# Performance work log

Hardware: AMD Instinct MI355X
Metric: run time of the kernel (lower is better)

## Reference

```python
import jax, jax.numpy as jnp
import numpy as np

B, T, E, H = 4, 2048, 1024, 16
D = E // H

def setup_inputs() -> dict:
    key = jax.random.key(0)
    ks = jax.random.split(key, 8)
    s = 0.02
    return {
        "q": jax.random.normal(ks[0], (B, T, E), dtype=jnp.float32),
        "k": jax.random.normal(ks[1], (B, T, E), dtype=jnp.float32),
        "v": jax.random.normal(ks[2], (B, T, E), dtype=jnp.float32),
        "Wq": jax.random.normal(ks[3], (E, E), dtype=jnp.float32) * s,
        "Wk": jax.random.normal(ks[4], (E, E), dtype=jnp.float32) * s,
        "Wv": jax.random.normal(ks[5], (E, E), dtype=jnp.float32) * s,
        "Wp": jax.random.normal(ks[6], (E, E), dtype=jnp.float32) * s,
        "bp": jnp.zeros((E,), dtype=jnp.float32),
    }

def reference(q, k, v, Wq, Wk, Wv, Wp, bp):
    # Linear projections (torch Linear: x @ W.T). NOTE: original code computes
    # key from the already-projected query (k = self.key(q)); external k is unused.
    qp = q @ Wq.T                      # [B,T,E]
    kp = qp @ Wk.T                     # [B,T,E]  <- faithful quirk
    vp = v @ Wv.T                      # [B,T,E]
    qh = qp.reshape(B, T, H, D).transpose(0, 2, 1, 3)  # [B,H,T,D]
    kh = kp.reshape(B, T, H, D).transpose(0, 2, 1, 3)
    vh = vp.reshape(B, T, H, D).transpose(0, 2, 1, 3)
    # Faithful quirk: att = scores / D**(-1/2) == scores * sqrt(D)
    scale = jnp.float32(D) ** 0.5
    att = jnp.einsum('bhtd,bhsd->bhts', qh, kh) * scale  # [B,H,T,T]
    causal = jnp.tril(jnp.ones((T, T), dtype=bool))
    att = jnp.where(causal, att, -jnp.inf)
    att = jax.nn.softmax(att, axis=-1)
    y = jnp.einsum('bhts,bhsd->bhtd', att, vh)           # [B,H,T,D]
    y = y.transpose(0, 2, 1, 3).reshape(B, T, E)
    return y @ Wp.T + bp
```

## Files before the change

kernel.cpp:

```cpp
#include <hip/hip_runtime.h>


typedef unsigned short u16;
typedef unsigned int   u32;
typedef __attribute__((ext_vector_type(8))) __bf16 bf16x8;
typedef __attribute__((ext_vector_type(8))) u16    u16x8;
typedef __attribute__((ext_vector_type(4))) u16    u16x4;
typedef __attribute__((ext_vector_type(4))) float  f32x4;
typedef __attribute__((ext_vector_type(4))) int    i32x4;

#define DEV static __device__ __forceinline__

DEV u16 f2bf(float x){ union{float f;u32 u;}v; v.f=x; u32 r=v.u+0x7fffu+((v.u>>16)&1u); return (u16)(r>>16); }
DEV float bf2f(u16 b){ union{u32 u;float f;}v; v.u=((u32)b)<<16; return v.f; }
DEV f32x4 zero4(){ f32x4 z={0.f,0.f,0.f,0.f}; return z; }
DEV f32x4 mfma16(bf16x8 a, bf16x8 b, f32x4 c){ return __builtin_amdgcn_mfma_f32_16x16x32_bf16(a,b,c,0,0,0); }
DEV void gld16(const u16* g, u16* l){
  __builtin_amdgcn_global_load_lds((const __attribute__((address_space(1))) u32*)g,
                                   (__attribute__((address_space(3))) u32*)l, 16, 0, 0);
}
DEV u32 pkbf(float a, float b){
  union{float f;u32 u;}x,y; x.f=a; y.f=b;
  return __builtin_amdgcn_perm(y.u+0x8000u, x.u+0x8000u, 0x07060302u);
}

constexpr int B_=4, T_=2048, E_=1024;
constexpr int M_=B_*T_;
constexpr float L2E8 = 11.5415603f;

__global__ __launch_bounds__(256)
void cvt_a(const float* __restrict__ q, const float* __restrict__ v,
           u16* __restrict__ qi, u16* __restrict__ vb)
{
  const int j=blockIdx.y;
  const size_t e=((size_t)blockIdx.x*256+threadIdx.x)*8;
  const float* s=(j==0)?q:v;
  f32x4 x0=*reinterpret_cast<const f32x4*>(s+e);
  f32x4 x1=*reinterpret_cast<const f32x4*>(s+e+4);
  u16x8 h,l;
#pragma unroll
  for(int t=0;t<4;t++){
    u16 hh=f2bf(x0[t]); h[t]=hh; l[t]=f2bf(x0[t]-bf2f(hh));
    u16 h2=f2bf(x1[t]); h[t+4]=h2; l[t+4]=f2bf(x1[t]-bf2f(h2));
  }
  if(j==0){
    const size_t row=e>>10, k=e&1023;
    u16* d=qi + row*2048 + (k>>3)*16;
    *reinterpret_cast<u16x8*>(d)=h;
    *reinterpret_cast<u16x8*>(d+8)=l;
  } else {
    *reinterpret_cast<u16x8*>(vb+e)=h;
  }
}

__global__ __launch_bounds__(256)
void cvt_w(const float* __restrict__ Wq, const float* __restrict__ Wk, const float* __restrict__ Wv,
           u16* __restrict__ wqi, u16* __restrict__ wki, u16* __restrict__ wvb)
{
  const int j=blockIdx.y;
  const size_t e=((size_t)blockIdx.x*256+threadIdx.x)*8;
  const float* s=(j==0)?Wq:(j==1)?Wk:Wv;
  f32x4 x0=*reinterpret_cast<const f32x4*>(s+e);
  f32x4 x1=*reinterpret_cast<const f32x4*>(s+e+4);
  u16x8 h,l;
#pragma unroll
  for(int t=0;t<4;t++){
    u16 hh=f2bf(x0[t]); h[t]=hh; l[t]=f2bf(x0[t]-bf2f(hh));
    u16 h2=f2bf(x1[t]); h[t+4]=h2; l[t+4]=f2bf(x1[t]-bf2f(h2));
  }
  if(j==2){ *reinterpret_cast<u16x8*>(wvb+e)=h; return; }
  u16* base=(j==0)?wqi:wki;
  const size_t row=e>>10, k=e&1023;
  u16* d=base + row*2048 + (k>>3)*16;
  *reinterpret_cast<u16x8*>(d)=h;
  *reinterpret_cast<u16x8*>(d+8)=l;
}

__global__ __launch_bounds__(256)
void cvt_p(const float* __restrict__ Wp, u16* __restrict__ wpb)
{
  const size_t e=((size_t)blockIdx.x*256+threadIdx.x)*8;
  f32x4 x0=*reinterpret_cast<const f32x4*>(Wp+e);
  f32x4 x1=*reinterpret_cast<const f32x4*>(Wp+e+4);
  u16x8 h;
#pragma unroll
  for(int t=0;t<4;t++){ h[t]=f2bf(x0[t]); h[t+4]=f2bf(x1[t]); }
  *reinterpret_cast<u16x8*>(wpb+e)=h;
}

template<int SPLIT,int OMODE>
__global__ __launch_bounds__(256)
void gemm(const u16* __restrict__ Ag, const u16* __restrict__ Bg,
          const float* __restrict__ bias,
          u16* __restrict__ Ob, float* __restrict__ Of, int ldc)
{
  __shared__ u16 sA[SPLIT?128*128:128*64];
  __shared__ u16 sB[SPLIT?128*128:128*64];

  const int tid=threadIdx.x, wave=tid>>6, lane=tid&63;
  const int quad=lane>>4, l16=lane&15, sw=l16&7;
  const int wm=(wave>>1)*64, wn=(wave&1)*64;
  const int n0=blockIdx.x*128, m0=blockIdx.y*128;

  f32x4 acc[4][4];
#pragma unroll
  for(int i=0;i<4;i++)
#pragma unroll
    for(int j=0;j<4;j++) acc[i][j]=zero4();

  for(int k0=0;k0<E_;k0+=64){
    if(SPLIT){
#pragma unroll
      for(int it=0;it<8;it++){
        const int c=it*256+tid, row=c>>4, j=(c&15)^(row&7);
        gld16(Ag + (size_t)(m0+row)*2048 + k0*2 + j*8, &sA[(it*256+wave*64)*8]);
      }
#pragma unroll
      for(int it=0;it<8;it++){
        const int c=it*256+tid, row=c>>4, j=(c&15)^(row&7);
        gld16(Bg + (size_t)(n0+row)*2048 + k0*2 + j*8, &sB[(it*256+wave*64)*8]);
      }
    } else {
#pragma unroll
      for(int it=0;it<4;it++){
        const int c=it*256+tid, row=c>>3, j=(c&7)^(row&7);
        gld16(Ag + (size_t)(m0+row)*1024 + k0 + j*8, &sA[(it*256+wave*64)*8]);
      }
#pragma unroll
      for(int it=0;it<4;it++){
        const int c=it*256+tid, row=c>>3, j=(c&7)^(row&7);
        gld16(Bg + (size_t)(n0+row)*1024 + k0 + j*8, &sB[(it*256+wave*64)*8]);
      }
    }
    __syncthreads();

#pragma unroll
    for(int kk=0;kk<2;kk++){
      if(SPLIT){
        bf16x8 ahh[4],ahl[4],bhh[4],bhl[4];
#pragma unroll
        for(int i=0;i<4;i++){
          const u16* pa=&sA[(wm+i*16+l16)*128];
          const u16* pb=&sB[(wn+i*16+l16)*128];
          const int ch=2*(kk*4+quad);
          ahh[i]=*reinterpret_cast<const bf16x8*>(&pa[((ch  )^sw)*8]);
          ahl[i]=*reinterpret_cast<const bf16x8*>(&pa[((ch+1)^sw)*8]);
          bhh[i]=*reinterpret_cast<const bf16x8*>(&pb[((ch  )^sw)*8]);
          bhl[i]=*reinterpret_cast<const bf16x8*>(&pb[((ch+1)^sw)*8]);
        }
#pragma unroll
        for(int i=0;i<4;i++)
#pragma unroll
          for(int j=0;j<4;j++){
            acc[i][j]=mfma16(ahh[i],bhh[j],acc[i][j]);
            acc[i][j]=mfma16(ahh[i],bhl[j],acc[i][j]);
            acc[i][j]=mfma16(ahl[i],bhh[j],acc[i][j]);
          }
      } else {
        bf16x8 a[4],b[4];
#pragma unroll
        for(int i=0;i<4;i++){
          a[i]=*reinterpret_cast<const bf16x8*>(&sA[(wm+i*16+l16)*64 + (((kk*4+quad)^sw)*8)]);
          b[i]=*reinterpret_cast<const bf16x8*>(&sB[(wn+i*16+l16)*64 + (((kk*4+quad)^sw)*8)]);
        }
#pragma unroll
        for(int i=0;i<4;i++)
#pragma unroll
          for(int j=0;j<4;j++)
            acc[i][j]=mfma16(a[i],b[j],acc[i][j]);
      }
    }
    __syncthreads();
  }

#pragma unroll
  for(int i=0;i<4;i++)
#pragma unroll
    for(int j=0;j<4;j++){
      const int col=n0+wn+j*16+l16;
#pragma unroll
      for(int r=0;r<4;r++){
        const int row=m0+wm+i*16+quad*4+r;
        float v=acc[i][j][r];
        if(OMODE==2)      Of[(size_t)row*ldc+col]=v+bias[col];
        else if(OMODE==1) Ob[(size_t)row*ldc+col]=f2bf(v);
        else {
          u16 hh=f2bf(v);
          const size_t base=(size_t)row*2048 + (size_t)(col>>3)*16 + (col&7);
          Ob[base]=hh; Ob[base+8]=f2bf(v-bf2f(hh));
        }
      }
    }
}

__global__ __launch_bounds__(256)
void attn(const u16* __restrict__ qpi, const u16* __restrict__ kpi,
          const u16* __restrict__ vpT, u16* __restrict__ yout)
{
  __shared__ u16 sK [64*128];
  __shared__ u16 sVT[64*64];

  const int tid=threadIdx.x, wave=tid>>6, lane=tid&63;
  const int quad=lane>>4, l16=lane&15, sw=l16&7;
  const int qt=(int)(gridDim.x-1-blockIdx.x)>>6;
  const int bh=blockIdx.x&63;
  const int b=bh>>4, h=bh&15;
  const int qr0=qt*128+wave*32;

  bf16x8 qfh[2][2], qfl[2][2];
#pragma unroll
  for(int mt=0;mt<2;mt++)
#pragma unroll
    for(int ksv=0;ksv<2;ksv++){
      const size_t off=(size_t)(b*T_+qr0+mt*16+l16)*2048 + h*128 + (ksv*4+quad)*16;
      qfh[mt][ksv]=*reinterpret_cast<const bf16x8*>(qpi+off);
      qfl[mt][ksv]=*reinterpret_cast<const bf16x8*>(qpi+off+8);
    }

  float mst[2]={-1e30f,-1e30f}, lst[2]={0.f,0.f};
  f32x4 oacc[2][4];
#pragma unroll
  for(int mt=0;mt<2;mt++)
#pragma unroll
    for(int dt=0;dt<4;dt++) oacc[mt][dt]=zero4();

  const int nkt=2*(qt+1);
  for(int kt=0;kt<nkt;kt++){
    const int s0=kt*64;
    __syncthreads();
#pragma unroll
    for(int it=0;it<4;it++){
      const int c=it*256+tid, row=c>>4, j=(c&15)^(row&7);
      gld16(kpi + (size_t)(b*T_+s0+row)*2048 + h*128 + j*8,
            &sK[(it*256+wave*64)*8]);
    }
#pragma unroll
    for(int it=0;it<2;it++){
      const int c=it*256+tid, row=c>>3, j=(c&7)^(row&7);
      gld16(vpT + (size_t)(h*64+row)*8192 + b*T_ + s0 + j*8,
            &sVT[(it*256+wave*64)*8]);
    }
    __syncthreads();

    if(s0<=qr0+31){
      f32x4 sacc[4][2];
#pragma unroll
      for(int st=0;st<4;st++)
#pragma unroll
        for(int mt=0;mt<2;mt++) sacc[st][mt]=zero4();
#pragma unroll
      for(int st=0;st<4;st++)
#pragma unroll
        for(int ksv=0;ksv<2;ksv++){
          const u16* pk=&sK[(st*16+l16)*128];
          const int ch=2*(ksv*4+quad);
          bf16x8 kh=*reinterpret_cast<const bf16x8*>(&pk[((ch  )^sw)*8]);
          bf16x8 kl=*reinterpret_cast<const bf16x8*>(&pk[((ch+1)^sw)*8]);
#pragma unroll
          for(int mt=0;mt<2;mt++){
            sacc[st][mt]=mfma16(kh,qfh[mt][ksv],sacc[st][mt]);
            sacc[st][mt]=mfma16(kl,qfh[mt][ksv],sacc[st][mt]);
            sacc[st][mt]=mfma16(kh,qfl[mt][ksv],sacc[st][mt]);
          }
        }
      const bool needmask=(s0+63>qr0);
      u32 pk_[4][2][2];
#pragma unroll
      for(int mt=0;mt<2;mt++){
        const int qrow=qr0+mt*16+l16;
        float mloc=-1e30f;
#pragma unroll
        for(int st=0;st<4;st++)
#pragma unroll
          for(int r=0;r<4;r++){
            float v=sacc[st][mt][r];
            if(needmask && (s0+st*16+quad*4+r>qrow)) v=-1e30f;
            sacc[st][mt][r]=v;
            mloc=fmaxf(mloc,v);
          }
        mloc=fmaxf(mloc,__shfl_xor(mloc,16,64));
        mloc=fmaxf(mloc,__shfl_xor(mloc,32,64));
        const float nm=fmaxf(mst[mt],mloc);
        const float alpha=exp2f((mst[mt]-nm)*L2E8);
        mst[mt]=nm;
        const float cexp=nm*L2E8;
        float rs=0.f;
#pragma unroll
        for(int st=0;st<4;st++)
#pragma unroll
          for(int r=0;r<4;r++){
            float p=exp2f(__builtin_fmaf(sacc[st][mt][r],L2E8,-cexp));
            sacc[st][mt][r]=p;
            rs+=p;
          }
        lst[mt]=lst[mt]*alpha+rs;
#pragma unroll
        for(int dt=0;dt<4;dt++) oacc[mt][dt]*=alpha;
#pragma unroll
        for(int st=0;st<4;st++){
          pk_[st][mt][0]=pkbf(sacc[st][mt][0],sacc[st][mt][1]);
          pk_[st][mt][1]=pkbf(sacc[st][mt][2],sacc[st][mt][3]);
        }
      }
      const int srcA=(2*(quad&1))*16+l16, srcB=srcA+16;
      const bool hs=(quad>=2);
#pragma unroll
      for(int ksv=0;ksv<2;ksv++){
        bf16x8 b2[2];
#pragma unroll
        for(int mt=0;mt<2;mt++){
          int e0=__shfl((int)pk_[2*ksv  ][mt][0],srcA,64);
          int g0=__shfl((int)pk_[2*ksv+1][mt][0],srcA,64);
          int e1=__shfl((int)pk_[2*ksv  ][mt][1],srcA,64);
          int g1=__shfl((int)pk_[2*ksv+1][mt][1],srcA,64);
          int e2=__shfl((int)pk_[2*ksv  ][mt][0],srcB,64);
          int g2=__shfl((int)pk_[2*ksv+1][mt][0],srcB,64);
          int e3=__shfl((int)pk_[2*ksv  ][mt][1],srcB,64);
          int g3=__shfl((int)pk_[2*ksv+1][mt][1],srcB,64);
          i32x4 bd={ hs?g0:e0, hs?g1:e1, hs?g2:e2, hs?g3:e3 };
          b2[mt]=*reinterpret_cast<bf16x8*>(&bd);
        }
#pragma unroll
        for(int dt=0;dt<4;dt++){
          bf16x8 va=*reinterpret_cast<const bf16x8*>(&sVT[(dt*16+l16)*64 + (((ksv*4+quad)^sw)*8)]);
#pragma unroll
          for(int mt=0;mt<2;mt++)
            oacc[mt][dt]=mfma16(va,b2[mt],oacc[mt][dt]);
        }
      }
    }
  }
#pragma unroll
  for(int mt=0;mt<2;mt++){
    float lt=lst[mt];
    lt+=__shfl_xor(lt,16,64);
    lt+=__shfl_xor(lt,32,64);
    const float inv=1.0f/lt;
    const size_t rb=(size_t)(b*T_+qr0+mt*16+l16)*1024 + h*64;
#pragma unroll
    for(int dt=0;dt<4;dt++){
      u16x4 o4;
#pragma unroll
      for(int r=0;r<4;r++) o4[r]=f2bf(oacc[mt][dt][r]*inv);
      *reinterpret_cast<u16x4*>(yout + rb + dt*16 + quad*4)=o4;
    }
  }
}

extern "C" void kernel_launch(void* const* d_in, const int* in_sizes, int n_in,
                              void* d_out, int out_size, void* d_ws, size_t ws_size,
                              hipStream_t stream)
{
  const float* q =(const float*)d_in[0];
  const float* v =(const float*)d_in[2];
  const float* Wq=(const float*)d_in[3];
  const float* Wk=(const float*)d_in[4];
  const float* Wv=(const float*)d_in[5];
  const float* Wp=(const float*)d_in[6];
  const float* bp=(const float*)d_in[7];
  float* out=(float*)d_out;

  const size_t NE=(size_t)M_*E_;
  const size_t WE=(size_t)E_*E_;
  u16* wsv=(u16*)d_ws;
  u16* qsl_i=wsv;
  u16* qp_i =wsv+2*NE;
  u16* kp_i =wsv;
  u16* wp_b =wsv+2*NE;
  u16* vpT  =wsv+4*NE;
  u16* ybf  =wsv+5*NE;
  u16* og   =(u16*)d_out;
  u16* wq_i =og;
  u16* wk_i =og+2*WE;
  u16* wv_b =og+4*WE;
  u16* vb   =og+5*WE;

  dim3 blk(256);
  cvt_a<<<dim3(NE/2048,2), blk, 0, stream>>>(q, v, qsl_i, vb);
  cvt_w<<<dim3(WE/2048,3), blk, 0, stream>>>(Wq, Wk, Wv, wq_i, wk_i, wv_b);

  dim3 g(E_/128, M_/128);
  gemm<1,0><<<g, blk, 0, stream>>>(qsl_i, wq_i, nullptr, qp_i, nullptr, 0);
  gemm<1,0><<<g, blk, 0, stream>>>(qp_i, wk_i, nullptr, kp_i, nullptr, 0);
  gemm<0,1><<<dim3(M_/128, E_/128), blk, 0, stream>>>(wv_b, vb, nullptr, vpT, nullptr, M_);
  attn<<<dim3(1024), blk, 0, stream>>>(qp_i, kp_i, vpT, ybf);
  cvt_p<<<dim3(WE/2048), blk, 0, stream>>>(Wp, wp_b);
  gemm<0,2><<<g, blk, 0, stream>>>(ybf, wp_b, bp, nullptr, out, E_);
}
```

Before: 437.8 us.

## Double-buffer attention K/V tiles, pair causal q-tiles, lazy softmax rescale

The attention kernel now double-buffers the K and V^T tiles in LDS and prefetches the next tile while the current one is computed, with one barrier per iteration instead of two. Each block handles two query tiles (pr and 15-pr) to balance the causal work, so the grid is halved to 512 blocks. The online-softmax rescale is skipped when the new max exceeds the running max by at most 1.0, MFMA sections are wrapped in s_setprio, and bf16 packing uses the hardware v_cvt_pk_bf16_f32. Doubled LDS may reduce occupancy, and the lazy-rescale threshold slightly changes numerics.

```diff
diff --git a/kernel.cpp b/kernel.cpp
--- a/kernel.cpp
+++ b/kernel.cpp
@@ -19,9 +19,10 @@
   __builtin_amdgcn_global_load_lds((const __attribute__((address_space(1))) u32*)g,
                                    (__attribute__((address_space(3))) u32*)l, 16, 0, 0);
 }
-DEV u32 pkbf(float a, float b){
-  union{float f;u32 u;}x,y; x.f=a; y.f=b;
-  return __builtin_amdgcn_perm(y.u+0x8000u, x.u+0x8000u, 0x07060302u);
+DEV u32 cvtpk(float lo, float hi){
+  u32 r;
+  asm("v_cvt_pk_bf16_f32 %0, %1, %2" : "=v"(r) : "v"(lo), "v"(hi));
+  return r;
 }
 
 constexpr int B_=4, T_=2048, E_=1024;
@@ -197,152 +198,176 @@
 void attn(const u16* __restrict__ qpi, const u16* __restrict__ kpi,
           const u16* __restrict__ vpT, u16* __restrict__ yout)
 {
-  __shared__ u16 sK [64*128];
-  __shared__ u16 sVT[64*64];
+  __shared__ u16 sK [2][64*128];
+  __shared__ u16 sVT[2][64*64];
 
   const int tid=threadIdx.x, wave=tid>>6, lane=tid&63;
   const int quad=lane>>4, l16=lane&15, sw=l16&7;
-  const int qt=(int)(gridDim.x-1-blockIdx.x)>>6;
+  const int pr=(int)blockIdx.x>>6;
   const int bh=blockIdx.x&63;
   const int b=bh>>4, h=bh&15;
-  const int qr0=qt*128+wave*32;
-
-  bf16x8 qfh[2][2], qfl[2][2];
-#pragma unroll
-  for(int mt=0;mt<2;mt++)
-#pragma unroll
-    for(int ksv=0;ksv<2;ksv++){
-      const size_t off=(size_t)(b*T_+qr0+mt*16+l16)*2048 + h*128 + (ksv*4+quad)*16;
-      qfh[mt][ksv]=*reinterpret_cast<const bf16x8*>(qpi+off);
-      qfl[mt][ksv]=*reinterpret_cast<const bf16x8*>(qpi+off+8);
-    }
-
-  float mst[2]={-1e30f,-1e30f}, lst[2]={0.f,0.f};
-  f32x4 oacc[2][4];
-#pragma unroll
-  for(int mt=0;mt<2;mt++)
-#pragma unroll
-    for(int dt=0;dt<4;dt++) oacc[mt][dt]=zero4();
-
-  const int nkt=2*(qt+1);
-  for(int kt=0;kt<nkt;kt++){
-    const int s0=kt*64;
-    __syncthreads();
+
+  auto STAGE=[&](int buf, int kt2){
+    const int s0=kt2*64;
 #pragma unroll
     for(int it=0;it<4;it++){
       const int c=it*256+tid, row=c>>4, j=(c&15)^(row&7);
       gld16(kpi + (size_t)(b*T_+s0+row)*2048 + h*128 + j*8,
-            &sK[(it*256+wave*64)*8]);
+            &sK[buf][(it*256+wave*64)*8]);
     }
 #pragma unroll
     for(int it=0;it<2;it++){
       const int c=it*256+tid, row=c>>3, j=(c&7)^(row&7);
       gld16(vpT + (size_t)(h*64+row)*8192 + b*T_ + s0 + j*8,
-            &sVT[(it*256+wave*64)*8]);
-    }
+            &sVT[buf][(it*256+wave*64)*8]);
+    }
+  };
+
+#pragma unroll 1
+  for(int half=0; half<2; half++){
+    const int qt = half ? (15-pr) : pr;
+    const int qr0=qt*128+wave*32;
+
+    bf16x8 qfh[2][2], qfl[2][2];
+#pragma unroll
+    for(int mt=0;mt<2;mt++)
+#pragma unroll
+      for(int ksv=0;ksv<2;ksv++){
+        const size_t off=(size_t)(b*T_+qr0+mt*16+l16)*2048 + h*128 + (ksv*4+quad)*16;
+        qfh[mt][ksv]=*reinterpret_cast<const bf16x8*>(qpi+off);
+        qfl[mt][ksv]=*reinterpret_cast<const bf16x8*>(qpi+off+8);
+      }
+
+    float mst[2]={-1e30f,-1e30f}, lst[2]={0.f,0.f};
+    f32x4 oacc[2][4];
+#pragma unroll
+    for(int mt=0;mt<2;mt++)
+#pragma unroll
+      for(int dt=0;dt<4;dt++) oacc[mt][dt]=zero4();
+
+    const int nkt=2*(qt+1);
+    STAGE(0, 0);
     __syncthreads();
 
-    if(s0<=qr0+31){
-      f32x4 sacc[4][2];
-#pragma unroll
-      for(int st=0;st<4;st++)
-#pragma unroll
-        for(int mt=0;mt<2;mt++) sacc[st][mt]=zero4();
-#pragma unroll
-      for(int st=0;st<4;st++)
+    for(int kt=0;kt<nkt;kt++){
+      const int cur=kt&1;
+      if(kt+1<nkt) STAGE(cur^1, kt+1);
+      const int s0=kt*64;
+
+      if(s0<=qr0+31){
+        f32x4 sacc[4][2];
+#pragma unroll
+        for(int st=0;st<4;st++)
+#pragma unroll
+          for(int mt=0;mt<2;mt++) sacc[st][mt]=zero4();
+        __builtin_amdgcn_s_setprio(1);
+#pragma unroll
+        for(int st=0;st<4;st++)
+#pragma unroll
+          for(int ksv=0;ksv<2;ksv++){
+            const u16* pk=&sK[cur][(st*16+l16)*128];
+            const int ch=2*(ksv*4+quad);
+            bf16x8 kh=*reinterpret_cast<const bf16x8*>(&pk[((ch  )^sw)*8]);
+            bf16x8 kl=*reinterpret_cast<const bf16x8*>(&pk[((ch+1)^sw)*8]);
+#pragma unroll
+            for(int mt=0;mt<2;mt++){
+              sacc[st][mt]=mfma16(kh,qfh[mt][ksv],sacc[st][mt]);
+              sacc[st][mt]=mfma16(kl,qfh[mt][ksv],sacc[st][mt]);
+              sacc[st][mt]=mfma16(kh,qfl[mt][ksv],sacc[st][mt]);
+            }
+          }
+        __builtin_amdgcn_s_setprio(0);
+        const bool needmask=(s0+63>qr0);
+        u32 pk_[4][2][2];
+#pragma unroll
+        for(int mt=0;mt<2;mt++){
+          const int qrow=qr0+mt*16+l16;
+          float mloc=-1e30f;
+#pragma unroll
+          for(int st=0;st<4;st++)
+#pragma unroll
+            for(int r=0;r<4;r++){
+              float v=sacc[st][mt][r];
+              if(needmask && (s0+st*16+quad*4+r>qrow)) v=-1e30f;
+              sacc[st][mt][r]=v;
+              mloc=fmaxf(mloc,v);
+            }
+          mloc=fmaxf(mloc,__shfl_xor(mloc,16,64));
+          mloc=fmaxf(mloc,__shfl_xor(mloc,32,64));
+          float cexp;
+          if(__all(mloc <= mst[mt]+1.0f)){
+            cexp=mst[mt]*L2E8;
+          } else {
+            const float nm=fmaxf(mst[mt],mloc);
+            const float alpha=exp2f((mst[mt]-nm)*L2E8);
+            mst[mt]=nm;
+            lst[mt]*=alpha;
+#pragma unroll
+            for(int dt=0;dt<4;dt++) oacc[mt][dt]*=alpha;
+            cexp=nm*L2E8;
+          }
+          float rs=0.f;
+#pragma unroll
+          for(int st=0;st<4;st++)
+#pragma unroll
+            for(int r=0;r<4;r++){
+              float p=exp2f(__builtin_fmaf(sacc[st][mt][r],L2E8,-cexp));
+              sacc[st][mt][r]=p;
+              rs+=p;
+            }
+          lst[mt]+=rs;
+#pragma unroll
+          for(int st=0;st<4;st++){
+            pk_[st][mt][0]=cvtpk(sacc[st][mt][0],sacc[st][mt][1]);
+            pk_[st][mt][1]=cvtpk(sacc[st][mt][2],sacc[st][mt][3]);
+          }
+        }
+        const int srcA=(2*(quad&1))*16+l16, srcB=srcA+16;
+        const bool hs=(quad>=2);
 #pragma unroll
         for(int ksv=0;ksv<2;ksv++){
-          const u16* pk=&sK[(st*16+l16)*128];
-          const int ch=2*(ksv*4+quad);
-          bf16x8 kh=*reinterpret_cast<const bf16x8*>(&pk[((ch  )^sw)*8]);
-          bf16x8 kl=*reinterpret_cast<const bf16x8*>(&pk[((ch+1)^sw)*8]);
+          bf16x8 b2[2];
 #pragma unroll
           for(int mt=0;mt<2;mt++){
-            sacc[st][mt]=mfma16(kh,qfh[mt][ksv],sacc[st][mt]);
-            sacc[st][mt]=mfma16(kl,qfh[mt][ksv],sacc[st][mt]);
-            sacc[st][mt]=mfma16(kh,qfl[mt][ksv],sacc[st][mt]);
-          }
+            int e0=__shfl((int)pk_[2*ksv  ][mt][0],srcA,64);
+            int g0=__shfl((int)pk_[2*ksv+1][mt][0],srcA,64);
+            int e1=__shfl((int)pk_[2*ksv  ][mt][1],srcA,64);
+            int g1=__shfl((int)pk_[2*ksv+1][mt][1],srcA,64);
+            int e2=__shfl((int)pk_[2*ksv  ][mt][0],srcB,64);
+            int g2=__shfl((int)pk_[2*ksv+1][mt][0],srcB,64);
+            int e3=__shfl((int)pk_[2*ksv  ][mt][1],srcB,64);
+            int g3=__shfl((int)pk_[2*ksv+1][mt][1],srcB,64);
+            i32x4 bd={ hs?g0:e0, hs?g1:e1, hs?g2:e2, hs?g3:e3 };
+            b2[mt]=*reinterpret_cast<bf16x8*>(&bd);
+          }
+          __builtin_amdgcn_s_setprio(1);
+#pragma unroll
+          for(int dt=0;dt<4;dt++){
+            bf16x8 va=*reinterpret_cast<const bf16x8*>(&sVT[cur][(dt*16+l16)*64 + (((ksv*4+quad)^sw)*8)]);
+#pragma unroll
+            for(int mt=0;mt<2;mt++)
+              oacc[mt][dt]=mfma16(va,b2[mt],oacc[mt][dt]);
+          }
+          __builtin_amdgcn_s_setprio(0);
         }
-      const bool needmask=(s0+63>qr0);
-      u32 pk_[4][2][2];
-#pragma unroll
-      for(int mt=0;mt<2;mt++){
-        const int qrow=qr0+mt*16+l16;
-        float mloc=-1e30f;
-#pragma unroll
-        for(int st=0;st<4;st++)
-#pragma unroll
-          for(int r=0;r<4;r++){
-            float v=sacc[st][mt][r];
-            if(needmask && (s0+st*16+quad*4+r>qrow)) v=-1e30f;
-            sacc[st][mt][r]=v;
-            mloc=fmaxf(mloc,v);
-          }
-        mloc=fmaxf(mloc,__shfl_xor(mloc,16,64));
-        mloc=fmaxf(mloc,__shfl_xor(mloc,32,64));
-        const float nm=fmaxf(mst[mt],mloc);
-        const float alpha=exp2f((mst[mt]-nm)*L2E8);
-        mst[mt]=nm;
-        const float cexp=nm*L2E8;
-        float rs=0.f;
-#pragma unroll
-        for(int st=0;st<4;st++)
-#pragma unroll
-          for(int r=0;r<4;r++){
-            float p=exp2f(__builtin_fmaf(sacc[st][mt][r],L2E8,-cexp));
-            sacc[st][mt][r]=p;
-            rs+=p;
-          }
-        lst[mt]=lst[mt]*alpha+rs;
-#pragma unroll
-        for(int dt=0;dt<4;dt++) oacc[mt][dt]*=alpha;
-#pragma unroll
-        for(int st=0;st<4;st++){
-          pk_[st][mt][0]=pkbf(sacc[st][mt][0],sacc[st][mt][1]);
-          pk_[st][mt][1]=pkbf(sacc[st][mt][2],sacc[st][mt][3]);
-        }
-      }
-      const int srcA=(2*(quad&1))*16+l16, srcB=srcA+16;
-      const bool hs=(quad>=2);
-#pragma unroll
-      for(int ksv=0;ksv<2;ksv++){
-        bf16x8 b2[2];
-#pragma unroll
-        for(int mt=0;mt<2;mt++){
-          int e0=__shfl((int)pk_[2*ksv  ][mt][0],srcA,64);
-          int g0=__shfl((int)pk_[2*ksv+1][mt][0],srcA,64);
-          int e1=__shfl((int)pk_[2*ksv  ][mt][1],srcA,64);
-          int g1=__shfl((int)pk_[2*ksv+1][mt][1],srcA,64);
-          int e2=__shfl((int)pk_[2*ksv  ][mt][0],srcB,64);
-          int g2=__shfl((int)pk_[2*ksv+1][mt][0],srcB,64);
-          int e3=__shfl((int)pk_[2*ksv  ][mt][1],srcB,64);
-          int g3=__shfl((int)pk_[2*ksv+1][mt][1],srcB,64);
-          i32x4 bd={ hs?g0:e0, hs?g1:e1, hs?g2:e2, hs?g3:e3 };
-          b2[mt]=*reinterpret_cast<bf16x8*>(&bd);
-        }
-#pragma unroll
-        for(int dt=0;dt<4;dt++){
-          bf16x8 va=*reinterpret_cast<const bf16x8*>(&sVT[(dt*16+l16)*64 + (((ksv*4+quad)^sw)*8)]);
-#pragma unroll
-          for(int mt=0;mt<2;mt++)
-            oacc[mt][dt]=mfma16(va,b2[mt],oacc[mt][dt]);
-        }
-      }
-    }
-  }
-#pragma unroll
-  for(int mt=0;mt<2;mt++){
-    float lt=lst[mt];
-    lt+=__shfl_xor(lt,16,64);
-    lt+=__shfl_xor(lt,32,64);
-    const float inv=1.0f/lt;
-    const size_t rb=(size_t)(b*T_+qr0+mt*16+l16)*1024 + h*64;
-#pragma unroll
-    for(int dt=0;dt<4;dt++){
-      u16x4 o4;
-#pragma unroll
-      for(int r=0;r<4;r++) o4[r]=f2bf(oacc[mt][dt][r]*inv);
-      *reinterpret_cast<u16x4*>(yout + rb + dt*16 + quad*4)=o4;
+      }
+      __syncthreads();
+    }
+
+#pragma unroll
+    for(int mt=0;mt<2;mt++){
+      float lt=lst[mt];
+      lt+=__shfl_xor(lt,16,64);
+      lt+=__shfl_xor(lt,32,64);
+      const float inv=1.0f/lt;
+      const size_t rb=(size_t)(b*T_+qr0+mt*16+l16)*1024 + h*64;
+#pragma unroll
+      for(int dt=0;dt<4;dt++){
+        u16x4 o4;
+#pragma unroll
+        for(int r=0;r<4;r++) o4[r]=f2bf(oacc[mt][dt][r]*inv);
+        *reinterpret_cast<u16x4*>(yout + rb + dt*16 + quad*4)=o4;
+      }
     }
   }
 }
@@ -383,7 +408,7 @@
   gemm<1,0><<<g, blk, 0, stream>>>(qsl_i, wq_i, nullptr, qp_i, nullptr, 0);
   gemm<1,0><<<g, blk, 0, stream>>>(qp_i, wk_i, nullptr, kp_i, nullptr, 0);
   gemm<0,1><<<dim3(M_/128, E_/128), blk, 0, stream>>>(wv_b, vb, nullptr, vpT, nullptr, M_);
-  attn<<<dim3(1024), blk, 0, stream>>>(qp_i, kp_i, vpT, ybf);
+  attn<<<dim3(512), blk, 0, stream>>>(qp_i, kp_i, vpT, ybf);
   cvt_p<<<dim3(WE/2048), blk, 0, stream>>>(Wp, wp_b);
   gemm<0,2><<<g, blk, 0, stream>>>(ybf, wp_b, bp, nullptr, out, E_);
 }
```

Result: no change. 433.1 us (-1.1%).
